# Kernel tuning notes

Measured on AMD Instinct MI355X. Metric: run time of the kernel, lower is better.

## Reference

```python
import jax, jax.numpy as jnp
import numpy as np

N = 512
H = 128
L = 4
NUM_RBF = 50
CUTOFF = 5.0
NMOL = 16
OUT = 1


def setup_inputs() -> dict:
    key = jax.random.key(0)
    ks = jax.random.split(key, 12)
    s = lambda f: 1.0 / np.sqrt(f)
    atomic_numbers = jax.random.randint(ks[0], (N,), 0, 100)
    positions = jax.random.normal(ks[1], (N, 3), dtype=jnp.float32) * 2.0
    batch = jnp.sort(jax.random.randint(ks[2], (N,), 0, NMOL))
    return {
        'atomic_numbers': atomic_numbers,
        'positions': positions,
        'batch': batch,
        'embed': jax.random.normal(ks[3], (100, H), dtype=jnp.float32) * 0.1,
        'msg_w1': jax.random.normal(ks[4], (L, H + NUM_RBF + 3, H), dtype=jnp.float32) * s(H + NUM_RBF + 3),
        'msg_b1': jnp.zeros((L, H), jnp.float32),
        'msg_w2': jax.random.normal(ks[5], (L, H, H), dtype=jnp.float32) * s(H),
        'msg_b2': jnp.zeros((L, H), jnp.float32),
        'upd_w1': jax.random.normal(ks[6], (L, 2 * H, H), dtype=jnp.float32) * s(2 * H),
        'upd_b1': jnp.zeros((L, H), jnp.float32),
        'upd_w2': jax.random.normal(ks[7], (L, H, H), dtype=jnp.float32) * s(H),
        'upd_b2': jnp.zeros((L, H), jnp.float32),
        'out_w1': jax.random.normal(ks[8], (H, H // 2), dtype=jnp.float32) * s(H),
        'out_b1': jnp.zeros((H // 2,), jnp.float32),
        'out_w2': jax.random.normal(ks[9], (H // 2, OUT), dtype=jnp.float32) * s(H // 2),
        'out_b2': jnp.zeros((OUT,), jnp.float32),
    }


def _forward(atomic_numbers, positions, batch, embed, msg_w1, msg_b1, msg_w2,
             msg_b2, upd_w1, upd_b1, upd_w2, upd_b2, out_w1, out_b1, out_w2, out_b2):
    x = embed[jnp.clip(atomic_numbers, 0, 99)]                      # [N,H]
    # all-pairs geometry: row i = source, col j = target (matches repeat_interleave/repeat)
    diff = positions[:, None, :] - positions[None, :, :]            # [N,N,3]
    dist = jnp.linalg.norm(diff, axis=-1)                           # [N,N]
    not_self = jnp.arange(N)[:, None] != jnp.arange(N)[None, :]
    valid = (dist < CUTOFF) & not_self                              # [N,N] edge mask
    dirs = diff / jnp.maximum(dist, 1e-8)[..., None]                # [N,N,3]
    # gaussian RBF: centers linspace(0, cutoff, num_rbf), width = cutoff/num_rbf
    centers = jnp.linspace(0.0, CUTOFF, NUM_RBF)
    width = CUTOFF / NUM_RBF
    rbf = jnp.exp(-(dist[..., None] - centers) ** 2 / (2.0 * width ** 2))  # [N,N,50]

    for l in range(L):
        # Linear over concat([x_j, rbf, dirs]) split by input blocks (same math)
        Wx = msg_w1[l, :H]
        Wr = msg_w1[l, H:H + NUM_RBF]
        Wd = msg_w1[l, H + NUM_RBF:]
        pre = (x @ Wx)[:, None, :] \
            + jnp.einsum('ijr,rh->ijh', rbf, Wr) \
            + jnp.einsum('ijd,dh->ijh', dirs, Wd) + msg_b1[l]       # [N,N,H]
        m = jax.nn.silu(pre) @ msg_w2[l] + msg_b2[l]                # [N,N,H]
        m = jnp.where(valid[..., None], m, 0.0)
        aggr = m.sum(axis=0)                                        # scatter-add to target j
        upd_in = jnp.concatenate([x, aggr], axis=-1)                # [N,2H]
        x = x + jax.nn.silu(upd_in @ upd_w1[l] + upd_b1[l]) @ upd_w2[l] + upd_b2[l]

    # per-molecule mean pool
    sums = jax.ops.segment_sum(x, batch, num_segments=NMOL)         # [NMOL,H]
    counts = jax.ops.segment_sum(jnp.ones((N,), x.dtype), batch, num_segments=NMOL)
    pooled = sums / jnp.maximum(counts, 1.0)[:, None]
    return jax.nn.silu(pooled @ out_w1 + out_b1) @ out_w2 + out_b2  # [NMOL,OUT]


def reference(atomic_numbers, positions, batch, embed, msg_w1, msg_b1, msg_w2,
              msg_b2, upd_w1, upd_b1, upd_w2, upd_b2, out_w1, out_b1, out_w2, out_b2):
    return _forward(atomic_numbers, positions, batch, embed, msg_w1, msg_b1, msg_w2,
                    msg_b2, upd_w1, upd_b1, upd_w2, upd_b2, out_w1, out_b1, out_w2, out_b2)
```

## Files before the change

kernel.cpp:

```cpp
#include <hip/hip_runtime.h>
#include <math.h>

#define N 512
#define H 128
#define L 4
#define NUM_RBF 50
#define NMOL 16
#define SUPER 64
#define MAXS 8

typedef __attribute__((ext_vector_type(8))) short short8;
typedef __attribute__((ext_vector_type(4))) float float4v;
typedef __attribute__((ext_vector_type(4))) int int4v;

__device__ __forceinline__ float silu_f(float v) {
    return v * __builtin_amdgcn_rcpf(1.0f + __expf(-v));
}

__device__ __forceinline__ unsigned short f2bf(float f) {
    unsigned int u = __float_as_uint(f);
    unsigned int r = (u + 0x7FFFu + ((u >> 16) & 1u)) >> 16;
    return (unsigned short)r;
}

__device__ __forceinline__ void gld_lds16(const void* g, void* l) {
    __builtin_amdgcn_global_load_lds(
        (const __attribute__((address_space(1))) unsigned int*)g,
        (__attribute__((address_space(3))) unsigned int*)l, 16, 0, 0);
}

__global__ __launch_bounds__(512) void k_embed_lin(const int* __restrict__ an,
                                                   const float* __restrict__ embed,
                                                   const float* __restrict__ pos,
                                                   const float* __restrict__ wx,
                                                   const float* __restrict__ b1,
                                                   float* __restrict__ x,
                                                   float* __restrict__ a,
                                                   int* __restrict__ nbr,
                                                   int* __restrict__ ncnt,
                                                   unsigned short* __restrict__ Fg) {
    int j = blockIdx.x;
    int tid = threadIdx.x;
    int lane = tid & 63;
    int wave = tid >> 6;
    int h = tid & 127;
    int grp = tid >> 7;

    __shared__ float xs[H];
    __shared__ int wsum8[8];
    __shared__ float part[4][H];

    float pjx = pos[j * 3 + 0], pjy = pos[j * 3 + 1], pjz = pos[j * 3 + 2];

    if (tid < H) {
        int z = an[j];
        z = min(max(z, 0), 99);
        float xv = embed[z * H + tid];
        xs[tid] = xv;
        x[j * H + tid] = xv;
    }

    int padded;
    {
        int i = tid;
        float dx = pos[i * 3 + 0] - pjx;
        float dy = pos[i * 3 + 1] - pjy;
        float dz = pos[i * 3 + 2] - pjz;
        float d2 = dx * dx + dy * dy + dz * dz;
        int valid = (d2 < 25.0f) && (i != j);
        unsigned long long m = __ballot(valid);
        int pre = __popcll(m & ((1ull << lane) - 1ull));
        if (lane == 0) wsum8[wave] = __popcll(m);
        __syncthreads();
        int wbase = 0, total = 0;
        for (int w = 0; w < 8; w++) {
            if (w < wave) wbase += wsum8[w];
            total += wsum8[w];
        }
        if (valid) nbr[j * 512 + wbase + pre] = i;
        padded = (total + 63) & ~63;
        for (int s = total + tid; s < padded; s += 512) nbr[j * 512 + s] = j;
        if (tid == 0) ncnt[j] = total;
    }

    {
        float p0 = 0.f, p1 = 0.f, p2 = 0.f, p3 = 0.f;
        int k0 = grp * 32;
#pragma unroll 8
        for (int k = 0; k < 32; k += 4) {
            p0 += xs[k0 + k]     * wx[(k0 + k)     * H + h];
            p1 += xs[k0 + k + 1] * wx[(k0 + k + 1) * H + h];
            p2 += xs[k0 + k + 2] * wx[(k0 + k + 2) * H + h];
            p3 += xs[k0 + k + 3] * wx[(k0 + k + 3) * H + h];
        }
        part[grp][h] = (p0 + p1) + (p2 + p3);
    }
    __syncthreads();
    if (grp == 0)
        a[j * H + h] = part[0][h] + part[1][h] + part[2][h] + part[3][h] + b1[h];

    const float DELTA = 5.0f / 49.0f;
    int kb = (tid & 3) * 16;
#pragma unroll
    for (int pass = 0; pass < 4; pass++) {
        int slot = pass * 128 + (tid >> 2);
        if (slot < padded) {
            int ni = nbr[j * 512 + slot];
            float dx = pos[ni * 3 + 0] - pjx;
            float dy = pos[ni * 3 + 1] - pjy;
            float dz = pos[ni * 3 + 2] - pjz;
            float d = sqrtf(dx * dx + dy * dy + dz * dz);
            float rinv = 1.0f / fmaxf(d, 1e-8f);
            unsigned short vals[16];
#pragma unroll
            for (int qq = 0; qq < 16; qq++) {
                int k = kb + qq;
                float v;
                if (k < NUM_RBF) {
                    float tt = d - (float)k * DELTA;
                    v = __expf(-50.0f * tt * tt);
                } else if (k == NUM_RBF)     v = dx * rinv;
                else if (k == NUM_RBF + 1)   v = dy * rinv;
                else if (k == NUM_RBF + 2)   v = dz * rinv;
                else                         v = 0.0f;
                vals[qq] = f2bf(v);
            }
            int row = slot & 63;
            unsigned short* tile = Fg + (((size_t)(j * MAXS + (slot >> 6))) << 12);
            int c0 = kb >> 3;
            int4v p0, p1;
#pragma unroll
            for (int q = 0; q < 4; q++) {
                p0[q] = (int)((unsigned)vals[2 * q]     | ((unsigned)vals[2 * q + 1] << 16));
                p1[q] = (int)((unsigned)vals[8 + 2 * q] | ((unsigned)vals[9 + 2 * q] << 16));
            }
            *(int4v*)(tile + row * 64 + (((c0    ) ^ (row & 7)) << 3)) = p0;
            *(int4v*)(tile + row * 64 + (((c0 + 1) ^ (row & 7)) << 3)) = p1;
        }
    }
}

__global__ __launch_bounds__(512) void k_layer(const float* __restrict__ a,
                                               const int* __restrict__ nbr,
                                               const int* __restrict__ ncnt,
                                               const unsigned short* __restrict__ Fg,
                                               const float* __restrict__ wfeat,
                                               const float* __restrict__ w2,
                                               const float* __restrict__ b2,
                                               const float* __restrict__ u1,
                                               const float* __restrict__ ub1,
                                               const float* __restrict__ u2,
                                               const float* __restrict__ ub2,
                                               float* __restrict__ x,
                                               const float* __restrict__ wxn,
                                               const float* __restrict__ b1n,
                                               float* __restrict__ a_next,
                                               const int* __restrict__ order_in,
                                               int* __restrict__ order_out) {
    int b = blockIdx.x;
    int tid = threadIdx.x;
    int g = tid >> 8;
    int lane = tid & 63;
    int wv4 = (tid >> 6) & 3;
    int nn = lane & 15;
    int quad = lane >> 4;
    int hbase = wv4 * 32;

    __shared__ __align__(16) unsigned short F[2][2][SUPER * 64];
    __shared__ __align__(16) int nidx_all[512];
    __shared__ __align__(16) int cnts_l[512];
    __shared__ int order_l[512];
    __shared__ float sjp[2][H];
    __shared__ float sj[H], xj[H], ag[H], hid[H], xn[H];
    __shared__ float part[4][H];

    int rank = (b < 256) ? b : 767 - b;
    int j;
    if (order_in != nullptr) {
        j = order_in[rank];
    } else {
        cnts_l[tid] = ncnt[tid];
        __syncthreads();
        int c_t = cnts_l[tid];
        int r = 0;
#pragma unroll 4
        for (int i = 0; i < 512; i += 4) {
            int4v c4 = *(const int4v*)&cnts_l[i];
            r += (c4[0] < c_t || (c4[0] == c_t && (i    ) < tid)) ? 1 : 0;
            r += (c4[1] < c_t || (c4[1] == c_t && (i + 1) < tid)) ? 1 : 0;
            r += (c4[2] < c_t || (c4[2] == c_t && (i + 2) < tid)) ? 1 : 0;
            r += (c4[3] < c_t || (c4[3] == c_t && (i + 3) < tid)) ? 1 : 0;
        }
        order_l[r] = tid;
        __syncthreads();
        j = order_l[rank];
        if (order_out != nullptr && b == 0) order_out[tid] = order_l[tid];
    }

    int cnt = ncnt[j];

    if (tid < 2 * H) sjp[tid >> 7][tid & 127] = 0.0f;
    if (tid < H) xj[tid] = x[j * H + tid];
    nidx_all[tid] = nbr[j * 512 + tid];

    short8 bfrag[2][2];
    for (int c = 0; c < 2; c++) {
        for (int t = 0; t < 2; t++) {
            short8 bb;
            int h = hbase + 16 * t + nn;
#pragma unroll
            for (int jj = 0; jj < 8; jj++) {
                int k = c * 32 + quad * 8 + jj;
                float v = (k < NUM_RBF + 3) ? wfeat[k * H + h] : 0.0f;
                bb[jj] = (short)f2bf(v);
            }
            bfrag[c][t] = bb;
        }
    }

    int S = (cnt + 63) >> 6;
    int rounds = (S + 1) >> 1;

    auto stage_tile = [&](int s, int buf) {
        const char* src = (const char*)(Fg + (((size_t)(j * MAXS + s)) << 12));
        char* dst = (char*)&F[g][buf][0];
#pragma unroll
        for (int q = 0; q < 2; q++) {
            int off = (wv4 + 4 * q) << 10;
            gld_lds16(src + off + lane * 16, dst + off);
        }
    };

    if (g < S) stage_tile(g, 0);
    __syncthreads();

    float pacc0 = 0.0f, pacc1 = 0.0f;

    for (int r = 0; r < rounds; r++) {
        int s = 2 * r + g;
        int sn = 2 * (r + 1) + g;
        if (sn < S) stage_tile(sn, (r + 1) & 1);
        if (s < S) {
            int cur = r & 1;
#pragma unroll
            for (int it = 0; it < SUPER / 16; it++) {
                int lbase = it * 16 + quad * 4;
                int4v ni4 = *(const int4v*)&nidx_all[s * 64 + lbase];
                float av0[4], av1[4];
#pragma unroll
                for (int rr = 0; rr < 4; rr++) {
                    av0[rr] = a[ni4[rr] * H + hbase + nn];
                    av1[rr] = a[ni4[rr] * H + hbase + 16 + nn];
                }
                int row = it * 16 + nn;
                const char* fb = (const char*)&F[g][cur][0] + row * 128;
                short8 afrag0 = *(const short8*)(fb + ((quad       ^ (row & 7)) << 4));
                short8 afrag1 = *(const short8*)(fb + (((quad + 4) ^ (row & 7)) << 4));
                float4v acc0 = {0.0f, 0.0f, 0.0f, 0.0f};
                float4v acc1 = {0.0f, 0.0f, 0.0f, 0.0f};
                acc0 = __builtin_amdgcn_mfma_f32_16x16x32_bf16(afrag0, bfrag[0][0], acc0, 0, 0, 0);
                acc0 = __builtin_amdgcn_mfma_f32_16x16x32_bf16(afrag1, bfrag[1][0], acc0, 0, 0, 0);
                acc1 = __builtin_amdgcn_mfma_f32_16x16x32_bf16(afrag0, bfrag[0][1], acc1, 0, 0, 0);
                acc1 = __builtin_amdgcn_mfma_f32_16x16x32_bf16(afrag1, bfrag[1][1], acc1, 0, 0, 0);
#pragma unroll
                for (int rr = 0; rr < 4; rr++) {
                    float vm = (s * 64 + lbase + rr < cnt) ? 1.0f : 0.0f;
                    pacc0 += vm * silu_f(acc0[rr] + av0[rr]);
                    pacc1 += vm * silu_f(acc1[rr] + av1[rr]);
                }
            }
        }
        __syncthreads();
    }

    pacc0 += __shfl_xor(pacc0, 16, 64);
    pacc0 += __shfl_xor(pacc0, 32, 64);
    pacc1 += __shfl_xor(pacc1, 16, 64);
    pacc1 += __shfl_xor(pacc1, 32, 64);
    if (lane < 16) {
        sjp[g][hbase + lane]      = pacc0;
        sjp[g][hbase + 16 + lane] = pacc1;
    }
    __syncthreads();
    if (tid < H) sj[tid] = sjp[0][tid] + sjp[1][tid];
    __syncthreads();

    int h = tid & 127;
    int grp = tid >> 7;

    {
        float p0 = 0.f, p1 = 0.f, p2 = 0.f, p3 = 0.f;
        int k0 = grp * 32;
#pragma unroll 8
        for (int k = 0; k < 32; k += 4) {
            p0 += sj[k0 + k]     * w2[(k0 + k)     * H + h];
            p1 += sj[k0 + k + 1] * w2[(k0 + k + 1) * H + h];
            p2 += sj[k0 + k + 2] * w2[(k0 + k + 2) * H + h];
            p3 += sj[k0 + k + 3] * w2[(k0 + k + 3) * H + h];
        }
        part[grp][h] = (p0 + p1) + (p2 + p3);
    }
    __syncthreads();
    if (grp == 0) ag[h] = part[0][h] + part[1][h] + part[2][h] + part[3][h] + (float)cnt * b2[h];
    __syncthreads();

    {
        const float* src = (grp < 2) ? xj : ag;
        int sbase = (grp & 1) * 64;
        int k0 = grp * 64;
        float p0 = 0.f, p1 = 0.f, p2 = 0.f, p3 = 0.f;
#pragma unroll 8
        for (int k = 0; k < 64; k += 4) {
            p0 += src[sbase + k]     * u1[(k0 + k)     * H + h];
            p1 += src[sbase + k + 1] * u1[(k0 + k + 1) * H + h];
            p2 += src[sbase + k + 2] * u1[(k0 + k + 2) * H + h];
            p3 += src[sbase + k + 3] * u1[(k0 + k + 3) * H + h];
        }
        part[grp][h] = (p0 + p1) + (p2 + p3);
    }
    __syncthreads();
    if (grp == 0) hid[h] = silu_f(part[0][h] + part[1][h] + part[2][h] + part[3][h] + ub1[h]);
    __syncthreads();

    {
        float p0 = 0.f, p1 = 0.f, p2 = 0.f, p3 = 0.f;
        int k0 = grp * 32;
#pragma unroll 8
        for (int k = 0; k < 32; k += 4) {
            p0 += hid[k0 + k]     * u2[(k0 + k)     * H + h];
            p1 += hid[k0 + k + 1] * u2[(k0 + k + 1) * H + h];
            p2 += hid[k0 + k + 2] * u2[(k0 + k + 2) * H + h];
            p3 += hid[k0 + k + 3] * u2[(k0 + k + 3) * H + h];
        }
        part[grp][h] = (p0 + p1) + (p2 + p3);
    }
    __syncthreads();
    if (grp == 0) {
        float xv = xj[h] + part[0][h] + part[1][h] + part[2][h] + part[3][h] + ub2[h];
        x[j * H + h] = xv;
        xn[h] = xv;
    }

    if (a_next != nullptr) {
        __syncthreads();
        float p0 = 0.f, p1 = 0.f, p2 = 0.f, p3 = 0.f;
        int k0 = grp * 32;
#pragma unroll 8
        for (int k = 0; k < 32; k += 4) {
            p0 += xn[k0 + k]     * wxn[(k0 + k)     * H + h];
            p1 += xn[k0 + k + 1] * wxn[(k0 + k + 1) * H + h];
            p2 += xn[k0 + k + 2] * wxn[(k0 + k + 2) * H + h];
            p3 += xn[k0 + k + 3] * wxn[(k0 + k + 3) * H + h];
        }
        part[grp][h] = (p0 + p1) + (p2 + p3);
        __syncthreads();
        if (grp == 0)
            a_next[j * H + h] = part[0][h] + part[1][h] + part[2][h] + part[3][h] + b1n[h];
    }
}

__global__ __launch_bounds__(512) void k_pool(const float* __restrict__ x,
                                              const int* __restrict__ batch,
                                              const float* __restrict__ ow1,
                                              const float* __restrict__ ob1,
                                              const float* __restrict__ ow2,
                                              const float* __restrict__ ob2,
                                              float* __restrict__ out) {
    int m = blockIdx.x;
    int tid = threadIdx.x;
    int h = tid & 127;
    int q = tid >> 7;
    __shared__ int lo_s, hi_s;
    __shared__ float psum[4][H];
    __shared__ float pooled[H];
    __shared__ float hid[H / 2];

    if (tid == 0) {
        int a = 0, b = N;
        while (a < b) { int mid = (a + b) >> 1; if (batch[mid] < m) a = mid + 1; else b = mid; }
        lo_s = a;
        b = N;
        while (a < b) { int mid = (a + b) >> 1; if (batch[mid] < m + 1) a = mid + 1; else b = mid; }
        hi_s = a;
    }
    __syncthreads();

    int lo = lo_s, hi = hi_s;
    float s = 0.0f;
    for (int i = lo + q; i < hi; i += 4) s += x[i * H + h];
    psum[q][h] = s;
    __syncthreads();
    if (q == 0) pooled[h] = (psum[0][h] + psum[1][h] + psum[2][h] + psum[3][h]) / (float)max(hi - lo, 1);
    __syncthreads();

    if (tid < H / 2) {
        float p0 = 0.f, p1 = 0.f;
        for (int k = 0; k < H; k += 2) {
            p0 += pooled[k]     * ow1[(k)     * (H / 2) + h];
            p1 += pooled[k + 1] * ow1[(k + 1) * (H / 2) + h];
        }
        hid[h] = silu_f(p0 + p1 + ob1[h]);
    }
    __syncthreads();

    if (tid == 0) {
        float o = ob2[0];
        for (int k = 0; k < H / 2; k++) o += hid[k] * ow2[k];
        out[m] = o;
    }
}

extern "C" void kernel_launch(void* const* d_in, const int* in_sizes, int n_in,
                              void* d_out, int out_size, void* d_ws, size_t ws_size,
                              hipStream_t stream) {
    const int*   an      = (const int*)d_in[0];
    const float* pos     = (const float*)d_in[1];
    const int*   batch   = (const int*)d_in[2];
    const float* embed   = (const float*)d_in[3];
    const float* msg_w1  = (const float*)d_in[4];
    const float* msg_b1  = (const float*)d_in[5];
    const float* msg_w2  = (const float*)d_in[6];
    const float* msg_b2  = (const float*)d_in[7];
    const float* upd_w1  = (const float*)d_in[8];
    const float* upd_b1  = (const float*)d_in[9];
    const float* upd_w2  = (const float*)d_in[10];
    const float* upd_b2  = (const float*)d_in[11];
    const float* out_w1  = (const float*)d_in[12];
    const float* out_b1  = (const float*)d_in[13];
    const float* out_w2  = (const float*)d_in[14];
    const float* out_b2  = (const float*)d_in[15];
    float* out = (float*)d_out;

    float* x    = (float*)d_ws;
    float* a0   = x + N * H;
    float* a1   = a0 + N * H;
    int*   nbr  = (int*)(a1 + N * H);
    int*   ncnt = nbr + N * 512;
    int*   order_g = ncnt + N;
    unsigned short* Fg = (unsigned short*)(order_g + N);

    const int W1ROWS = H + NUM_RBF + 3;

    k_embed_lin<<<N, 512, 0, stream>>>(an, embed, pos, msg_w1, msg_b1, x, a0, nbr, ncnt, Fg);
    for (int l = 0; l < L; l++) {
        float* a_cur  = (l & 1) ? a1 : a0;
        float* a_next = (l + 1 < L) ? ((l & 1) ? a0 : a1) : nullptr;
        const float* wxn = (l + 1 < L) ? (msg_w1 + (l + 1) * W1ROWS * H) : nullptr;
        const float* b1n = (l + 1 < L) ? (msg_b1 + (l + 1) * H) : nullptr;
        const int* oin  = (l == 0) ? nullptr : order_g;
        int*       oout = (l == 0) ? order_g : nullptr;
        k_layer<<<N, 512, 0, stream>>>(a_cur, nbr, ncnt, Fg,
                                       msg_w1 + l * W1ROWS * H + H * H,
                                       msg_w2 + l * H * H, msg_b2 + l * H,
                                       upd_w1 + l * 2 * H * H, upd_b1 + l * H,
                                       upd_w2 + l * H * H, upd_b2 + l * H,
                                       x, wxn, b1n, a_next, oin, oout);
    }
    k_pool<<<NMOL, 512, 0, stream>>>(x, batch, out_w1, out_b1, out_w2, out_b2, out);
}
```

Baseline: 201.3 us.

## Store edge features in MFMA fragment order and read directly from global

The edge-feature tiles are now written in the exact per-lane MFMA A-fragment layout, so k_layer loads fragments straight from global memory. This removes the LDS double-buffered staging with its barriers and the neighbour-index LDS copy. The RBF weight B-fragments are also pre-packed into bf16 fragment order once in the embed kernel, instead of being converted from fp32 in every layer block. The trade-off is that fragment loads no longer have async prefetch, so global latency may be exposed, in exchange for fewer synchronisations and smaller LDS use.

```diff
diff --git a/kernel.cpp b/kernel.cpp
--- a/kernel.cpp
+++ b/kernel.cpp
@@ -23,22 +23,17 @@
     return (unsigned short)r;
 }
 
-__device__ __forceinline__ void gld_lds16(const void* g, void* l) {
-    __builtin_amdgcn_global_load_lds(
-        (const __attribute__((address_space(1))) unsigned int*)g,
-        (__attribute__((address_space(3))) unsigned int*)l, 16, 0, 0);
-}
-
 __global__ __launch_bounds__(512) void k_embed_lin(const int* __restrict__ an,
                                                    const float* __restrict__ embed,
                                                    const float* __restrict__ pos,
-                                                   const float* __restrict__ wx,
+                                                   const float* __restrict__ msg_w1,
                                                    const float* __restrict__ b1,
                                                    float* __restrict__ x,
                                                    float* __restrict__ a,
                                                    int* __restrict__ nbr,
                                                    int* __restrict__ ncnt,
-                                                   unsigned short* __restrict__ Fg) {
+                                                   unsigned short* __restrict__ Fg,
+                                                   unsigned short* __restrict__ Wpack) {
     int j = blockIdx.x;
     int tid = threadIdx.x;
     int lane = tid & 63;
@@ -88,10 +83,10 @@
         int k0 = grp * 32;
 #pragma unroll 8
         for (int k = 0; k < 32; k += 4) {
-            p0 += xs[k0 + k]     * wx[(k0 + k)     * H + h];
-            p1 += xs[k0 + k + 1] * wx[(k0 + k + 1) * H + h];
-            p2 += xs[k0 + k + 2] * wx[(k0 + k + 2) * H + h];
-            p3 += xs[k0 + k + 3] * wx[(k0 + k + 3) * H + h];
+            p0 += xs[k0 + k]     * msg_w1[(k0 + k)     * H + h];
+            p1 += xs[k0 + k + 1] * msg_w1[(k0 + k + 1) * H + h];
+            p2 += xs[k0 + k + 2] * msg_w1[(k0 + k + 2) * H + h];
+            p3 += xs[k0 + k + 3] * msg_w1[(k0 + k + 3) * H + h];
         }
         part[grp][h] = (p0 + p1) + (p2 + p3);
     }
@@ -126,16 +121,41 @@
                 vals[qq] = f2bf(v);
             }
             int row = slot & 63;
+            int it = row >> 4, nn = row & 15;
             unsigned short* tile = Fg + (((size_t)(j * MAXS + (slot >> 6))) << 12);
-            int c0 = kb >> 3;
+            int fs = kb >> 5;
+            int q1 = (kb & 31) >> 3;
             int4v p0, p1;
 #pragma unroll
             for (int q = 0; q < 4; q++) {
                 p0[q] = (int)((unsigned)vals[2 * q]     | ((unsigned)vals[2 * q + 1] << 16));
                 p1[q] = (int)((unsigned)vals[8 + 2 * q] | ((unsigned)vals[9 + 2 * q] << 16));
             }
-            *(int4v*)(tile + row * 64 + (((c0    ) ^ (row & 7)) << 3)) = p0;
-            *(int4v*)(tile + row * 64 + (((c0 + 1) ^ (row & 7)) << 3)) = p1;
+            *(int4v*)(tile + (it * 64 + q1 * 16 + nn) * 16 + fs * 8)       = p0;
+            *(int4v*)(tile + (it * 64 + (q1 + 1) * 16 + nn) * 16 + fs * 8) = p1;
+        }
+    }
+
+    if (j < L) {
+        const float* wf = msg_w1 + j * (H + NUM_RBF + 3) * H + H * H;
+        unsigned short* wl = Wpack + j * 8192;
+        int wv4w = tid >> 7;
+        int rem = tid & 127;
+        int ln = rem >> 1;
+        int c = rem & 1;
+        int qd = ln >> 4, nnw = ln & 15;
+#pragma unroll
+        for (int t = 0; t < 2; t++) {
+            int hh = wv4w * 32 + t * 16 + nnw;
+            int4v pk;
+#pragma unroll
+            for (int q = 0; q < 4; q++) {
+                int k0 = c * 32 + qd * 8 + 2 * q;
+                float v0 = (k0     < NUM_RBF + 3) ? wf[(k0)     * H + hh] : 0.0f;
+                float v1 = (k0 + 1 < NUM_RBF + 3) ? wf[(k0 + 1) * H + hh] : 0.0f;
+                pk[q] = (int)((unsigned)f2bf(v0) | ((unsigned)f2bf(v1) << 16));
+            }
+            *(int4v*)(wl + ((wv4w * 64 + ln) * 4 + c * 2 + t) * 8) = pk;
         }
     }
 }
@@ -144,7 +164,7 @@
                                                const int* __restrict__ nbr,
                                                const int* __restrict__ ncnt,
                                                const unsigned short* __restrict__ Fg,
-                                               const float* __restrict__ wfeat,
+                                               const unsigned short* __restrict__ wpack,
                                                const float* __restrict__ w2,
                                                const float* __restrict__ b2,
                                                const float* __restrict__ u1,
@@ -166,8 +186,6 @@
     int quad = lane >> 4;
     int hbase = wv4 * 32;
 
-    __shared__ __align__(16) unsigned short F[2][2][SUPER * 64];
-    __shared__ __align__(16) int nidx_all[512];
     __shared__ __align__(16) int cnts_l[512];
     __shared__ int order_l[512];
     __shared__ float sjp[2][H];
@@ -199,78 +217,52 @@
 
     int cnt = ncnt[j];
 
-    if (tid < 2 * H) sjp[tid >> 7][tid & 127] = 0.0f;
     if (tid < H) xj[tid] = x[j * H + tid];
-    nidx_all[tid] = nbr[j * 512 + tid];
 
     short8 bfrag[2][2];
-    for (int c = 0; c < 2; c++) {
-        for (int t = 0; t < 2; t++) {
-            short8 bb;
-            int h = hbase + 16 * t + nn;
-#pragma unroll
-            for (int jj = 0; jj < 8; jj++) {
-                int k = c * 32 + quad * 8 + jj;
-                float v = (k < NUM_RBF + 3) ? wfeat[k * H + h] : 0.0f;
-                bb[jj] = (short)f2bf(v);
+    {
+        const unsigned short* wp = wpack + (wv4 * 64 + lane) * 32;
+        bfrag[0][0] = *(const short8*)(wp);
+        bfrag[0][1] = *(const short8*)(wp + 8);
+        bfrag[1][0] = *(const short8*)(wp + 16);
+        bfrag[1][1] = *(const short8*)(wp + 24);
+    }
+
+    int S = (cnt + 63) >> 6;
+
+    const float* ap = a + hbase + nn;
+    const unsigned short* tile0 = Fg + (((size_t)(j * MAXS)) << 12);
+
+    float pacc0 = 0.0f, pacc1 = 0.0f;
+
+    for (int s = g; s < S; s += 2) {
+        const unsigned short* tile = tile0 + ((size_t)s << 12);
+#pragma unroll
+        for (int it = 0; it < SUPER / 16; it++) {
+            int lbase = it * 16 + quad * 4;
+            int4v ni4 = *(const int4v*)&nbr[j * 512 + s * 64 + lbase];
+            float av0[4], av1[4];
+#pragma unroll
+            for (int rr = 0; rr < 4; rr++) {
+                av0[rr] = ap[ni4[rr] * H];
+                av1[rr] = ap[ni4[rr] * H + 16];
             }
-            bfrag[c][t] = bb;
-        }
-    }
-
-    int S = (cnt + 63) >> 6;
-    int rounds = (S + 1) >> 1;
-
-    auto stage_tile = [&](int s, int buf) {
-        const char* src = (const char*)(Fg + (((size_t)(j * MAXS + s)) << 12));
-        char* dst = (char*)&F[g][buf][0];
-#pragma unroll
-        for (int q = 0; q < 2; q++) {
-            int off = (wv4 + 4 * q) << 10;
-            gld_lds16(src + off + lane * 16, dst + off);
-        }
-    };
-
-    if (g < S) stage_tile(g, 0);
-    __syncthreads();
-
-    float pacc0 = 0.0f, pacc1 = 0.0f;
-
-    for (int r = 0; r < rounds; r++) {
-        int s = 2 * r + g;
-        int sn = 2 * (r + 1) + g;
-        if (sn < S) stage_tile(sn, (r + 1) & 1);
-        if (s < S) {
-            int cur = r & 1;
-#pragma unroll
-            for (int it = 0; it < SUPER / 16; it++) {
-                int lbase = it * 16 + quad * 4;
-                int4v ni4 = *(const int4v*)&nidx_all[s * 64 + lbase];
-                float av0[4], av1[4];
-#pragma unroll
-                for (int rr = 0; rr < 4; rr++) {
-                    av0[rr] = a[ni4[rr] * H + hbase + nn];
-                    av1[rr] = a[ni4[rr] * H + hbase + 16 + nn];
-                }
-                int row = it * 16 + nn;
-                const char* fb = (const char*)&F[g][cur][0] + row * 128;
-                short8 afrag0 = *(const short8*)(fb + ((quad       ^ (row & 7)) << 4));
-                short8 afrag1 = *(const short8*)(fb + (((quad + 4) ^ (row & 7)) << 4));
-                float4v acc0 = {0.0f, 0.0f, 0.0f, 0.0f};
-                float4v acc1 = {0.0f, 0.0f, 0.0f, 0.0f};
-                acc0 = __builtin_amdgcn_mfma_f32_16x16x32_bf16(afrag0, bfrag[0][0], acc0, 0, 0, 0);
-                acc0 = __builtin_amdgcn_mfma_f32_16x16x32_bf16(afrag1, bfrag[1][0], acc0, 0, 0, 0);
-                acc1 = __builtin_amdgcn_mfma_f32_16x16x32_bf16(afrag0, bfrag[0][1], acc1, 0, 0, 0);
-                acc1 = __builtin_amdgcn_mfma_f32_16x16x32_bf16(afrag1, bfrag[1][1], acc1, 0, 0, 0);
-#pragma unroll
-                for (int rr = 0; rr < 4; rr++) {
-                    float vm = (s * 64 + lbase + rr < cnt) ? 1.0f : 0.0f;
-                    pacc0 += vm * silu_f(acc0[rr] + av0[rr]);
-                    pacc1 += vm * silu_f(acc1[rr] + av1[rr]);
-                }
+            const unsigned short* fb = tile + (it * 64 + lane) * 16;
+            short8 afrag0 = *(const short8*)(fb);
+            short8 afrag1 = *(const short8*)(fb + 8);
+            float4v acc0 = {0.0f, 0.0f, 0.0f, 0.0f};
+            float4v acc1 = {0.0f, 0.0f, 0.0f, 0.0f};
+            acc0 = __builtin_amdgcn_mfma_f32_16x16x32_bf16(afrag0, bfrag[0][0], acc0, 0, 0, 0);
+            acc0 = __builtin_amdgcn_mfma_f32_16x16x32_bf16(afrag1, bfrag[1][0], acc0, 0, 0, 0);
+            acc1 = __builtin_amdgcn_mfma_f32_16x16x32_bf16(afrag0, bfrag[0][1], acc1, 0, 0, 0);
+            acc1 = __builtin_amdgcn_mfma_f32_16x16x32_bf16(afrag1, bfrag[1][1], acc1, 0, 0, 0);
+#pragma unroll
+            for (int rr = 0; rr < 4; rr++) {
+                float vm = (s * 64 + lbase + rr < cnt) ? 1.0f : 0.0f;
+                pacc0 += vm * silu_f(acc0[rr] + av0[rr]);
+                pacc1 += vm * silu_f(acc1[rr] + av1[rr]);
             }
         }
-        __syncthreads();
     }
 
     pacc0 += __shfl_xor(pacc0, 16, 64);
@@ -437,11 +429,12 @@
     int*   nbr  = (int*)(a1 + N * H);
     int*   ncnt = nbr + N * 512;
     int*   order_g = ncnt + N;
-    unsigned short* Fg = (unsigned short*)(order_g + N);
+    unsigned short* Wpack = (unsigned short*)(order_g + N);
+    unsigned short* Fg = Wpack + L * 8192;
 
     const int W1ROWS = H + NUM_RBF + 3;
 
-    k_embed_lin<<<N, 512, 0, stream>>>(an, embed, pos, msg_w1, msg_b1, x, a0, nbr, ncnt, Fg);
+    k_embed_lin<<<N, 512, 0, stream>>>(an, embed, pos, msg_w1, msg_b1, x, a0, nbr, ncnt, Fg, Wpack);
     for (int l = 0; l < L; l++) {
         float* a_cur  = (l & 1) ? a1 : a0;
         float* a_next = (l + 1 < L) ? ((l & 1) ? a0 : a1) : nullptr;
@@ -449,8 +442,7 @@
         const float* b1n = (l + 1 < L) ? (msg_b1 + (l + 1) * H) : nullptr;
         const int* oin  = (l == 0) ? nullptr : order_g;
         int*       oout = (l == 0) ? order_g : nullptr;
-        k_layer<<<N, 512, 0, stream>>>(a_cur, nbr, ncnt, Fg,
-                                       msg_w1 + l * W1ROWS * H + H * H,
+        k_layer<<<N, 512, 0, stream>>>(a_cur, nbr, ncnt, Fg, Wpack + l * 8192,
                                        msg_w2 + l * H * H, msg_b2 + l * H,
                                        upd_w1 + l * 2 * H * H, upd_b1 + l * H,
                                        upd_w2 + l * H * H, upd_b2 + l * H,
```

New measurement: 217.7 us. 1.08x slower.

## Prepack RBF weight fragments once and fuse pooling into last layer

Applied to the files above, without the earlier changes.

The RBF/direction weight B-fragments are converted to bf16 once in the embed kernel and stored pre-swizzled, so each layer block loads them with four vector loads instead of 64 scattered float loads and conversions. The separate pooling kernel is removed: in the final layer, the last block to finish (found through an atomic counter with threadfences) computes the per-molecule mean pool and output MLP. The sjp zeroing is also dropped. This removes one launch and some per-block setup, but the serial tail running on a single block may be slower than a 16-block pool kernel.

```diff
diff --git a/kernel.cpp b/kernel.cpp
--- a/kernel.cpp
+++ b/kernel.cpp
@@ -32,13 +32,15 @@
 __global__ __launch_bounds__(512) void k_embed_lin(const int* __restrict__ an,
                                                    const float* __restrict__ embed,
                                                    const float* __restrict__ pos,
-                                                   const float* __restrict__ wx,
+                                                   const float* __restrict__ msg_w1,
                                                    const float* __restrict__ b1,
                                                    float* __restrict__ x,
                                                    float* __restrict__ a,
                                                    int* __restrict__ nbr,
                                                    int* __restrict__ ncnt,
-                                                   unsigned short* __restrict__ Fg) {
+                                                   unsigned short* __restrict__ Fg,
+                                                   unsigned short* __restrict__ Wpack,
+                                                   int* __restrict__ done_g) {
     int j = blockIdx.x;
     int tid = threadIdx.x;
     int lane = tid & 63;
@@ -51,6 +53,8 @@
     __shared__ float part[4][H];
 
     float pjx = pos[j * 3 + 0], pjy = pos[j * 3 + 1], pjz = pos[j * 3 + 2];
+
+    if (j == 0 && tid == 0) *done_g = 0;
 
     if (tid < H) {
         int z = an[j];
@@ -88,10 +92,10 @@
         int k0 = grp * 32;
 #pragma unroll 8
         for (int k = 0; k < 32; k += 4) {
-            p0 += xs[k0 + k]     * wx[(k0 + k)     * H + h];
-            p1 += xs[k0 + k + 1] * wx[(k0 + k + 1) * H + h];
-            p2 += xs[k0 + k + 2] * wx[(k0 + k + 2) * H + h];
-            p3 += xs[k0 + k + 3] * wx[(k0 + k + 3) * H + h];
+            p0 += xs[k0 + k]     * msg_w1[(k0 + k)     * H + h];
+            p1 += xs[k0 + k + 1] * msg_w1[(k0 + k + 1) * H + h];
+            p2 += xs[k0 + k + 2] * msg_w1[(k0 + k + 2) * H + h];
+            p3 += xs[k0 + k + 3] * msg_w1[(k0 + k + 3) * H + h];
         }
         part[grp][h] = (p0 + p1) + (p2 + p3);
     }
@@ -138,13 +142,36 @@
             *(int4v*)(tile + row * 64 + (((c0 + 1) ^ (row & 7)) << 3)) = p1;
         }
     }
+
+    if (j < L) {
+        const float* wf = msg_w1 + j * (H + NUM_RBF + 3) * H + H * H;
+        unsigned short* wl = Wpack + j * 8192;
+        int wv4w = tid >> 7;
+        int rem = tid & 127;
+        int ln = rem >> 1;
+        int c = rem & 1;
+        int qd = ln >> 4, nnw = ln & 15;
+#pragma unroll
+        for (int t = 0; t < 2; t++) {
+            int hh = wv4w * 32 + t * 16 + nnw;
+            int4v pk;
+#pragma unroll
+            for (int q = 0; q < 4; q++) {
+                int k0 = c * 32 + qd * 8 + 2 * q;
+                float v0 = (k0     < NUM_RBF + 3) ? wf[(k0)     * H + hh] : 0.0f;
+                float v1 = (k0 + 1 < NUM_RBF + 3) ? wf[(k0 + 1) * H + hh] : 0.0f;
+                pk[q] = (int)((unsigned)f2bf(v0) | ((unsigned)f2bf(v1) << 16));
+            }
+            *(int4v*)(wl + ((wv4w * 64 + ln) * 4 + c * 2 + t) * 8) = pk;
+        }
+    }
 }
 
 __global__ __launch_bounds__(512) void k_layer(const float* __restrict__ a,
                                                const int* __restrict__ nbr,
                                                const int* __restrict__ ncnt,
                                                const unsigned short* __restrict__ Fg,
-                                               const float* __restrict__ wfeat,
+                                               const unsigned short* __restrict__ wpack,
                                                const float* __restrict__ w2,
                                                const float* __restrict__ b2,
                                                const float* __restrict__ u1,
@@ -156,7 +183,14 @@
                                                const float* __restrict__ b1n,
                                                float* __restrict__ a_next,
                                                const int* __restrict__ order_in,
-                                               int* __restrict__ order_out) {
+                                               int* __restrict__ order_out,
+                                               const int* __restrict__ batch,
+                                               const float* __restrict__ ow1,
+                                               const float* __restrict__ ob1,
+                                               const float* __restrict__ ow2,
+                                               const float* __restrict__ ob2,
+                                               float* __restrict__ out,
+                                               int* __restrict__ done_g) {
     int b = blockIdx.x;
     int tid = threadIdx.x;
     int g = tid >> 8;
@@ -173,6 +207,9 @@
     __shared__ float sjp[2][H];
     __shared__ float sj[H], xj[H], ag[H], hid[H], xn[H];
     __shared__ float part[4][H];
+    __shared__ int mlo[4], mhi[4];
+    __shared__ float phid[4][H / 2];
+    __shared__ int lastflag;
 
     int rank = (b < 256) ? b : 767 - b;
     int j;
@@ -199,23 +236,16 @@
 
     int cnt = ncnt[j];
 
-    if (tid < 2 * H) sjp[tid >> 7][tid & 127] = 0.0f;
     if (tid < H) xj[tid] = x[j * H + tid];
     nidx_all[tid] = nbr[j * 512 + tid];
 
     short8 bfrag[2][2];
-    for (int c = 0; c < 2; c++) {
-        for (int t = 0; t < 2; t++) {
-            short8 bb;
-            int h = hbase + 16 * t + nn;
-#pragma unroll
-            for (int jj = 0; jj < 8; jj++) {
-                int k = c * 32 + quad * 8 + jj;
-                float v = (k < NUM_RBF + 3) ? wfeat[k * H + h] : 0.0f;
-                bb[jj] = (short)f2bf(v);
-            }
-            bfrag[c][t] = bb;
-        }
+    {
+        const unsigned short* wp = wpack + (wv4 * 64 + lane) * 32;
+        bfrag[0][0] = *(const short8*)(wp);
+        bfrag[0][1] = *(const short8*)(wp + 8);
+        bfrag[1][0] = *(const short8*)(wp + 16);
+        bfrag[1][1] = *(const short8*)(wp + 24);
     }
 
     int S = (cnt + 63) >> 6;
@@ -356,57 +386,46 @@
         __syncthreads();
         if (grp == 0)
             a_next[j * H + h] = part[0][h] + part[1][h] + part[2][h] + part[3][h] + b1n[h];
-    }
-}
-
-__global__ __launch_bounds__(512) void k_pool(const float* __restrict__ x,
-                                              const int* __restrict__ batch,
-                                              const float* __restrict__ ow1,
-                                              const float* __restrict__ ob1,
-                                              const float* __restrict__ ow2,
-                                              const float* __restrict__ ob2,
-                                              float* __restrict__ out) {
-    int m = blockIdx.x;
-    int tid = threadIdx.x;
-    int h = tid & 127;
-    int q = tid >> 7;
-    __shared__ int lo_s, hi_s;
-    __shared__ float psum[4][H];
-    __shared__ float pooled[H];
-    __shared__ float hid[H / 2];
-
-    if (tid == 0) {
-        int a = 0, b = N;
-        while (a < b) { int mid = (a + b) >> 1; if (batch[mid] < m) a = mid + 1; else b = mid; }
-        lo_s = a;
-        b = N;
-        while (a < b) { int mid = (a + b) >> 1; if (batch[mid] < m + 1) a = mid + 1; else b = mid; }
-        hi_s = a;
-    }
-    __syncthreads();
-
-    int lo = lo_s, hi = hi_s;
-    float s = 0.0f;
-    for (int i = lo + q; i < hi; i += 4) s += x[i * H + h];
-    psum[q][h] = s;
-    __syncthreads();
-    if (q == 0) pooled[h] = (psum[0][h] + psum[1][h] + psum[2][h] + psum[3][h]) / (float)max(hi - lo, 1);
-    __syncthreads();
-
-    if (tid < H / 2) {
-        float p0 = 0.f, p1 = 0.f;
-        for (int k = 0; k < H; k += 2) {
-            p0 += pooled[k]     * ow1[(k)     * (H / 2) + h];
-            p1 += pooled[k + 1] * ow1[(k + 1) * (H / 2) + h];
-        }
-        hid[h] = silu_f(p0 + p1 + ob1[h]);
-    }
-    __syncthreads();
-
-    if (tid == 0) {
-        float o = ob2[0];
-        for (int k = 0; k < H / 2; k++) o += hid[k] * ow2[k];
-        out[m] = o;
+        return;
+    }
+
+    __syncthreads();
+    __threadfence();
+    if (tid == 0) lastflag = (atomicAdd(done_g, 1) == N - 1);
+    __syncthreads();
+    if (!lastflag) return;
+    __threadfence();
+
+    for (int m = grp; m < NMOL; m += 4) {
+        if (h == 0) {
+            int a_ = 0, b_ = N;
+            while (a_ < b_) { int mid = (a_ + b_) >> 1; if (batch[mid] < m) a_ = mid + 1; else b_ = mid; }
+            mlo[grp] = a_;
+            b_ = N;
+            while (a_ < b_) { int mid = (a_ + b_) >> 1; if (batch[mid] < m + 1) a_ = mid + 1; else b_ = mid; }
+            mhi[grp] = a_;
+        }
+        __syncthreads();
+        int lo = mlo[grp], hi = mhi[grp];
+        float s = 0.0f;
+        for (int i = lo; i < hi; i++) s += x[i * H + h];
+        part[grp][h] = s / (float)max(hi - lo, 1);
+        __syncthreads();
+        if (h < H / 2) {
+            float p0 = 0.f, p1 = 0.f;
+            for (int k = 0; k < H; k += 2) {
+                p0 += part[grp][k]     * ow1[(k)     * (H / 2) + h];
+                p1 += part[grp][k + 1] * ow1[(k + 1) * (H / 2) + h];
+            }
+            phid[grp][h] = silu_f(p0 + p1 + ob1[h]);
+        }
+        __syncthreads();
+        if (h == 0) {
+            float o = ob2[0];
+            for (int k = 0; k < H / 2; k++) o += phid[grp][k] * ow2[k];
+            out[m] = o;
+        }
+        __syncthreads();
     }
 }
 
@@ -437,11 +456,14 @@
     int*   nbr  = (int*)(a1 + N * H);
     int*   ncnt = nbr + N * 512;
     int*   order_g = ncnt + N;
-    unsigned short* Fg = (unsigned short*)(order_g + N);
+    int*   done_g  = order_g + N;
+    unsigned short* Wpack = (unsigned short*)(done_g + 4);
+    unsigned short* Fg = Wpack + L * 8192;
 
     const int W1ROWS = H + NUM_RBF + 3;
 
-    k_embed_lin<<<N, 512, 0, stream>>>(an, embed, pos, msg_w1, msg_b1, x, a0, nbr, ncnt, Fg);
+    k_embed_lin<<<N, 512, 0, stream>>>(an, embed, pos, msg_w1, msg_b1, x, a0,
+                                       nbr, ncnt, Fg, Wpack, done_g);
     for (int l = 0; l < L; l++) {
         float* a_cur  = (l & 1) ? a1 : a0;
         float* a_next = (l + 1 < L) ? ((l & 1) ? a0 : a1) : nullptr;
@@ -449,12 +471,12 @@
         const float* b1n = (l + 1 < L) ? (msg_b1 + (l + 1) * H) : nullptr;
         const int* oin  = (l == 0) ? nullptr : order_g;
         int*       oout = (l == 0) ? order_g : nullptr;
-        k_layer<<<N, 512, 0, stream>>>(a_cur, nbr, ncnt, Fg,
-                                       msg_w1 + l * W1ROWS * H + H * H,
+        k_layer<<<N, 512, 0, stream>>>(a_cur, nbr, ncnt, Fg, Wpack + l * 8192,
                                        msg_w2 + l * H * H, msg_b2 + l * H,
                                        upd_w1 + l * 2 * H * H, upd_b1 + l * H,
                                        upd_w2 + l * H * H, upd_b2 + l * H,
-                                       x, wxn, b1n, a_next, oin, oout);
-    }
-    k_pool<<<NMOL, 512, 0, stream>>>(x, batch, out_w1, out_b1, out_w2, out_b2, out);
-}
+                                       x, wxn, b1n, a_next, oin, oout,
+                                       batch, out_w1, out_b1, out_w2, out_b2,
+                                       out, done_g);
+    }
+}
```

After: 353.6 us. 1.76x slower.
